# Kernel optimization log

Measured on AMD Instinct MI355X. Metric: run time of the kernel, lower is better.

The kernel has to match this reference:

```python
import jax, jax.numpy as jnp
import numpy as np

HEADS = 16
DIM_HEAD = 64
SCALE = DIM_HEAD ** -0.5
STEP = 0.6

def setup_inputs() -> dict:
    key = jax.random.key(0)
    ks = jax.random.split(key, 8)
    B, N, QD = 2, 2048, 1024
    M, CD = 1024, 768
    inner = HEADS * DIM_HEAD  # 1024
    return {
        "x": jax.random.normal(ks[0], (B, N, QD), jnp.float32),
        "context": jax.random.normal(ks[1], (B, M, CD), jnp.float32),
        "focused_attention_mask": jax.random.uniform(ks[2], (1, M, M), jnp.float32),
        "Wq": jax.random.normal(ks[3], (inner, QD), jnp.float32) * 0.02,
        "Wk": jax.random.normal(ks[4], (inner, CD), jnp.float32) * 0.02,
        "Wv": jax.random.normal(ks[5], (inner, CD), jnp.float32) * 0.02,
        "Wo": jax.random.normal(ks[6], (QD, inner), jnp.float32) * 0.02,
        "bo": jax.random.normal(ks[7], (QD,), jnp.float32) * 0.02,
    }

def _split_heads(t, h):
    b, n, hd = t.shape
    return t.reshape(b, n, h, hd // h).transpose(0, 2, 1, 3).reshape(b * h, n, hd // h)

def reference(x, context, focused_attention_mask, Wq, Wk, Wv, Wo, bo):
    b, n, _ = x.shape
    h = HEADS
    q = _split_heads(x @ Wq.T, h)        # (b h) n d
    k = _split_heads(context @ Wk.T, h)  # (b h) m d
    v = _split_heads(context @ Wv.T, h)
    sim = jnp.einsum('bid,bjd->bij', q, k) * SCALE  # (b h) n m
    # FCA focus-weight modulation (fam has leading dim 1, broadcast over b*h)
    fam = focused_attention_mask[0]  # (m, m)
    K = fam.shape[-1]
    fw = jnp.abs(jnp.einsum('bqk,dk->bqd', sim[:, :, :K], fam))  # (b h) n m
    fw = jnp.minimum(fw, 1.0)
    fw = fw / (jnp.max(fw, axis=2, keepdims=True) + 1e-6)
    fw = (fw > STEP).astype(sim.dtype)
    sim = sim.at[:, :, :K].add((fw - 1.0) * 50.0)
    attn = jax.nn.softmax(sim, axis=-1)
    out = jnp.einsum('bij,bjd->bid', attn, v)  # (b h) n d
    out = out.reshape(b, h, n, -1).transpose(0, 2, 1, 3).reshape(b, n, -1)
    return out @ Wo.T + bo
```

## Files before the change

### kernel.cpp

```cpp
#include <hip/hip_runtime.h>
#include <hip/hip_fp16.h>
#include <math.h>

#define SCALE 0.125f

typedef _Float16 f16;
typedef __attribute__((ext_vector_type(8))) _Float16 f16x8;
typedef __attribute__((ext_vector_type(4))) float f32x4;

#define MFMA(a, b, c) __builtin_amdgcn_mfma_f32_16x16x32_f16((a), (b), (c), 0, 0, 0)

#define LX(r, qd) (((r) << 6) + ((((qd) ^ ((r) & 7))) << 3))

__device__ __forceinline__ void gll16(const f16* g, f16* l) {
    __builtin_amdgcn_global_load_lds(
        (const __attribute__((address_space(1))) unsigned int*)(g),
        (__attribute__((address_space(3))) unsigned int*)(l),
        16, 0, 0);
}

struct SplitSeg { const float* src; f16* h; f16* l; float scale; size_t n; };
struct SplitArgs { SplitSeg seg[7]; };

__global__ __launch_bounds__(256) void split_all(SplitArgs a)
{
    SplitSeg s = a.seg[blockIdx.y];
    size_t i4 = ((size_t)blockIdx.x * 256 + threadIdx.x) * 4;
    size_t stride = (size_t)gridDim.x * 256 * 4;
    for (; i4 < s.n; i4 += stride) {
        float4 v = *(const float4*)&s.src[i4];
        float av[4] = {v.x * s.scale, v.y * s.scale, v.z * s.scale, v.w * s.scale};
        f16 hv[4], lv[4];
#pragma unroll
        for (int j = 0; j < 4; ++j) {
            hv[j] = (f16)av[j];
            lv[j] = (f16)(av[j] - (float)hv[j]);
        }
        *(float2*)&s.h[i4] = *(float2*)hv;
        *(float2*)&s.l[i4] = *(float2*)lv;
    }
}

template <int AP, int BP>
__global__ __launch_bounds__(256) void gemm16(
    const f16* __restrict__ Ah, const f16* __restrict__ Al, size_t Abat,
    const f16* __restrict__ Bh, const f16* __restrict__ Bl, int Bstr, size_t Bbat,
    float* __restrict__ Cf, const float* __restrict__ bias,
    f16* __restrict__ Ch, f16* __restrict__ Cl, int Cpitch,
    f16* __restrict__ Cth, f16* __restrict__ Ctl, int Mt,
    int Nsplit, f16* __restrict__ C2th, int Mt2,
    size_t Cbat, float oscale, int M, int N, int K)
{
    constexpr int NCH = AP * 16 + BP * 8;
    __shared__ __align__(16) f16 Ash[AP][128 * 64];
    __shared__ __align__(16) f16 Bsh[BP][64 * 64];

    const int tid  = threadIdx.x;
    const int z    = blockIdx.z;
    Ah += z * Abat; if (AP == 2) Al += z * Abat;
    Bh += z * Bbat; if (BP == 2) Bl += z * Bbat;
    const int m0   = blockIdx.y * 128;
    const int n0   = blockIdx.x * 64;
    const int w    = tid >> 6;
    const int lane = tid & 63;
    const int wm   = (w >> 1) * 64;
    const int wn   = (w & 1) * 32;
    const int lq   = lane >> 4;
    const int l15  = lane & 15;
    const int sr   = lane >> 3;
    const int sg   = lane & 7;

    f32x4 acc[4][2];
#pragma unroll
    for (int mi = 0; mi < 4; ++mi)
#pragma unroll
        for (int ni = 0; ni < 2; ++ni) acc[mi][ni] = (f32x4){0.f, 0.f, 0.f, 0.f};

    for (int k0 = 0; k0 < K; k0 += 64) {
        __syncthreads();
#pragma unroll
        for (int c = 0; c < NCH / 4; ++c) {
            int chunk = c * 4 + w;
            const f16* gp; f16* lp;
            if (chunk < AP * 16) {
                int pl = chunk >> 4, sub = chunk & 15;
                int r = sub * 8 + sr;
                int g = sg ^ (r & 7);
                gp = ((AP == 2 && pl) ? Al : Ah) + (size_t)(m0 + r) * K + k0 + g * 8;
                lp = &Ash[pl][sub * 512];
            } else {
                int cb = chunk - AP * 16;
                int pl = cb >> 3, sub = cb & 7;
                int r = sub * 8 + sr;
                int g = sg ^ (r & 7);
                gp = ((BP == 2 && pl) ? Bl : Bh) + (size_t)(n0 + r) * Bstr + k0 + g * 8;
                lp = &Bsh[pl][sub * 512];
            }
            gll16(gp, lp);
        }
        __syncthreads();

#pragma unroll
        for (int kc = 0; kc < 2; ++kc) {
            f16x8 afh[4], afl[4];
#pragma unroll
            for (int mi = 0; mi < 4; ++mi) {
                int r = wm + mi * 16 + l15;
                afh[mi] = *(const f16x8*)&Ash[0][LX(r, kc * 4 + lq)];
                if (AP == 2) afl[mi] = *(const f16x8*)&Ash[1][LX(r, kc * 4 + lq)];
            }
#pragma unroll
            for (int ni = 0; ni < 2; ++ni) {
                int r = wn + ni * 16 + l15;
                f16x8 bh = *(const f16x8*)&Bsh[0][LX(r, kc * 4 + lq)];
                f16x8 bl;
                if (BP == 2) bl = *(const f16x8*)&Bsh[1][LX(r, kc * 4 + lq)];
#pragma unroll
                for (int mi = 0; mi < 4; ++mi) {
                    f32x4 a = acc[mi][ni];
                    a = MFMA(afh[mi], bh, a);
                    if (BP == 2) a = MFMA(afh[mi], bl, a);
                    if (AP == 2) a = MFMA(afl[mi], bh, a);
                    acc[mi][ni] = a;
                }
            }
        }
    }

    const bool vhalf = (Nsplit > 0) && (n0 >= Nsplit);
    if (Cf)  Cf  += z * Cbat;
    if (Ch)  { Ch += z * Cbat; if (Cl) Cl += z * Cbat; }

#pragma unroll
    for (int mi = 0; mi < 4; ++mi) {
#pragma unroll
        for (int ni = 0; ni < 2; ++ni) {
            int row = m0 + wm + mi * 16 + lq * 4;
            int col = n0 + wn + ni * 16 + l15;
            float v[4];
#pragma unroll
            for (int r = 0; r < 4; ++r) v[r] = acc[mi][ni][r] * oscale;
            if (Cf) {
                float bb = bias ? bias[col] : 0.f;
#pragma unroll
                for (int r = 0; r < 4; ++r)
                    Cf[(size_t)(row + r) * Cpitch + col] = v[r] + bb;
            } else if (vhalf) {
                union { f16 a[4]; float2 f; } uh;
#pragma unroll
                for (int r = 0; r < 4; ++r) uh.a[r] = (f16)v[r];
                *(float2*)&C2th[(size_t)(col - Nsplit) * Mt2 + row] = uh.f;
            } else {
                if (Ch) {
#pragma unroll
                    for (int r = 0; r < 4; ++r) {
                        f16 hh = (f16)v[r];
                        Ch[(size_t)(row + r) * Cpitch + col] = hh;
                        if (Cl) Cl[(size_t)(row + r) * Cpitch + col] = (f16)(v[r] - (float)hh);
                    }
                }
                if (Cth) {
                    union { f16 a[4]; float2 f; } uh, ul;
#pragma unroll
                    for (int r = 0; r < 4; ++r) {
                        uh.a[r] = (f16)v[r];
                        ul.a[r] = (f16)(v[r] - (float)uh.a[r]);
                    }
                    *(float2*)&Cth[(size_t)col * Mt + row] = uh.f;
                    if (Ctl) *(float2*)&Ctl[(size_t)col * Mt + row] = ul.f;
                }
            }
        }
    }
}

__global__ __launch_bounds__(512) void attn_mfma(
    const f16* __restrict__ Qh, const f16* __restrict__ Ql,
    const f16* __restrict__ Kh,
    const f16* __restrict__ Gh, const f16* __restrict__ Gl,
    const f16* __restrict__ Vth, f16* __restrict__ AOh)
{
    __shared__ __align__(16) f16 Ksh[2][4096];
    __shared__ __align__(16) f16 Gsh[2][2][4096];
    __shared__ __align__(16) f16 Vsh[4096];
    __shared__ __align__(16) f16 Ps[128 * 72];
    __shared__ int eflag[8];

    const int tid = threadIdx.x;
    const int bh = blockIdx.x;
    const int b = bh >> 4, h = bh & 15;
    const int qr0 = blockIdx.y * 128;
    const int w = tid >> 6, lane = tid & 63;
    const int lq = lane >> 4, l15 = lane & 15;
    const int wq = w * 16;

    const size_t qb = ((size_t)(b * 2048 + qr0)) * 1024 + h * 64;
    const size_t kb = ((size_t)(b * 1024)) * 1024 + h * 64;
    const size_t vb = (size_t)(h * 64) * 2048 + b * 1024;

    const int sr = lane >> 3;
    const int ss = lane & 7;

    f16x8 aqh[2], aql[2];
#pragma unroll
    for (int kc = 0; kc < 2; ++kc) {
        size_t off = qb + (size_t)(wq + l15) * 1024 + (kc * 4 + lq) * 8;
        aqh[kc] = *(const f16x8*)&Qh[off];
        aql[kc] = *(const f16x8*)&Ql[off];
    }

    float mx[4] = {};
    for (int jt = 0; jt < 16; ++jt) {
#pragma unroll
        for (int c = 0; c < 2; ++c) {
            int chunk = c * 8 + w;
            int pl = chunk >> 3, sub = chunk & 7;
            int r = sub * 8 + sr;
            int g = ss ^ (r & 7);
            const f16* gp = (pl ? Gl : Gh) + kb + (size_t)(jt * 64 + r) * 1024 + g * 8;
            gll16(gp, &Gsh[0][pl][sub * 512]);
        }
        __syncthreads();

#pragma unroll
        for (int tj = 0; tj < 4; ++tj) {
            f32x4 a0 = {0.f, 0.f, 0.f, 0.f};
#pragma unroll
            for (int kc = 0; kc < 2; ++kc) {
                int lx = LX(tj * 16 + l15, kc * 4 + lq);
                f16x8 bgh = *(const f16x8*)&Gsh[0][0][lx];
                f16x8 bgl = *(const f16x8*)&Gsh[0][1][lx];
                a0 = MFMA(aqh[kc], bgh, a0);
                a0 = MFMA(aqh[kc], bgl, a0);
                a0 = MFMA(aql[kc], bgh, a0);
            }
#pragma unroll
            for (int r = 0; r < 4; ++r)
                mx[r] = fmaxf(mx[r], fminf(fabsf(a0[r] * SCALE), 1.f));
        }
        bool done = true;
#pragma unroll
        for (int r = 0; r < 4; ++r) {
            float m = mx[r];
#pragma unroll
            for (int d = 1; d < 16; d <<= 1)
                m = fmaxf(m, __shfl_xor(m, d, 64));
            mx[r] = m;
            done = done && (m >= 1.0f);
        }
        int wd = __all(done ? 1 : 0);
        if (lane == 0) eflag[w] = wd;
        __syncthreads();
        bool allw = true;
#pragma unroll
        for (int i = 0; i < 8; ++i) allw = allw && (eflag[i] != 0);
        if (allw) break;
    }
    float T[4];
#pragma unroll
    for (int r = 0; r < 4; ++r)
        T[r] = 4.8f * (mx[r] + 1e-6f);

    const float SL2E = 0.125f * 1.44269504088896f;
    const float PEN2 = -50.0f * 1.44269504088896f;
    f32x4 aco[4];
#pragma unroll
    for (int dj = 0; dj < 4; ++dj) aco[dj] = (f32x4){0.f, 0.f, 0.f, 0.f};
    float dsum[4] = {};

    auto stageKG = [&](int jtn, int buf) {
#pragma unroll
        for (int c = 0; c < 3; ++c) {
            int chunk = c * 8 + w;
            int sub = chunk & 7;
            int r = sub * 8 + sr;
            int g = ss ^ (r & 7);
            size_t off = kb + (size_t)(jtn * 64 + r) * 1024 + g * 8;
            const f16* gp; f16* lp;
            if (chunk < 8)       { gp = Kh + off; lp = &Ksh[buf][sub * 512]; }
            else if (chunk < 16) { gp = Gh + off; lp = &Gsh[buf][0][sub * 512]; }
            else                 { gp = Gl + off; lp = &Gsh[buf][1][sub * 512]; }
            gll16(gp, lp);
        }
    };

    stageKG(0, 0);

    for (int jt = 0; jt < 16; ++jt) {
        const int cur = jt & 1;

        {
            int sub = w;
            int r = sub * 8 + sr;
            int g = ss ^ (r & 7);
            const f16* gp = Vth + vb + (size_t)r * 2048 + jt * 64 + g * 8;
            gll16(gp, &Vsh[sub * 512]);
        }
        if (jt < 15) {
            stageKG(jt + 1, cur ^ 1);
            asm volatile("s_waitcnt vmcnt(4)" ::: "memory");
        } else {
            asm volatile("s_waitcnt vmcnt(1)" ::: "memory");
        }
        __builtin_amdgcn_sched_barrier(0);
        __builtin_amdgcn_s_barrier();
        __builtin_amdgcn_sched_barrier(0);

#pragma unroll
        for (int tj = 0; tj < 4; ++tj) {
            f32x4 s0 = {0.f, 0.f, 0.f, 0.f}, f0 = {0.f, 0.f, 0.f, 0.f};
            __builtin_amdgcn_s_setprio(1);
#pragma unroll
            for (int kc = 0; kc < 2; ++kc) {
                int lx = LX(tj * 16 + l15, kc * 4 + lq);
                f16x8 bkh = *(const f16x8*)&Ksh[cur][lx];
                f16x8 bgh = *(const f16x8*)&Gsh[cur][0][lx];
                f16x8 bgl = *(const f16x8*)&Gsh[cur][1][lx];
                s0 = MFMA(aqh[kc], bkh, s0);
                f0 = MFMA(aqh[kc], bgh, f0);
                f0 = MFMA(aqh[kc], bgl, f0);
                f0 = MFMA(aql[kc], bgh, f0);
            }
            __builtin_amdgcn_s_setprio(0);
#pragma unroll
            for (int r = 0; r < 4; ++r) {
                float p0 = (fabsf(f0[r]) > T[r]) ? 0.f : PEN2;
                f16 e0 = (f16)exp2f(fmaf(s0[r], SL2E, p0));
                Ps[(wq + lq * 4 + r) * 72 + tj * 16 + l15] = e0;
                dsum[r] += (float)e0;
            }
        }

        if (jt < 15) asm volatile("s_waitcnt vmcnt(3)" ::: "memory");
        else         asm volatile("s_waitcnt vmcnt(0)" ::: "memory");
        asm volatile("s_waitcnt lgkmcnt(0)" ::: "memory");
        __builtin_amdgcn_sched_barrier(0);
        __builtin_amdgcn_s_barrier();
        __builtin_amdgcn_sched_barrier(0);

        __builtin_amdgcn_s_setprio(1);
#pragma unroll
        for (int kc = 0; kc < 2; ++kc) {
            f16x8 ap = *(const f16x8*)&Ps[(wq + l15) * 72 + kc * 32 + lq * 8];
#pragma unroll
            for (int dj = 0; dj < 4; ++dj) {
                int lx = LX(dj * 16 + l15, kc * 4 + lq);
                f16x8 bvh = *(const f16x8*)&Vsh[lx];
                aco[dj] = MFMA(ap, bvh, aco[dj]);
            }
        }
        __builtin_amdgcn_s_setprio(0);

        asm volatile("s_waitcnt lgkmcnt(0)" ::: "memory");
        __builtin_amdgcn_sched_barrier(0);
        __builtin_amdgcn_s_barrier();
        __builtin_amdgcn_sched_barrier(0);
    }

#pragma unroll
    for (int r = 0; r < 4; ++r) {
        float s = dsum[r];
#pragma unroll
        for (int d = 1; d < 16; d <<= 1)
            s += __shfl_xor(s, d, 64);
        dsum[r] = s;
    }
#pragma unroll
    for (int r = 0; r < 4; ++r) {
        float invd = 1.0f / dsum[r];
        int qq = qr0 + wq + lq * 4 + r;
#pragma unroll
        for (int dj = 0; dj < 4; ++dj) {
            int dd = h * 64 + dj * 16 + l15;
            AOh[(size_t)(b * 2048 + qq) * 1024 + dd] = (f16)(aco[dj][r] * invd);
        }
    }
}

extern "C" void kernel_launch(void* const* d_in, const int* in_sizes, int n_in,
                              void* d_out, int out_size, void* d_ws, size_t ws_size,
                              hipStream_t stream)
{
    const float* x   = (const float*)d_in[0];
    const float* ctx = (const float*)d_in[1];
    const float* fam = (const float*)d_in[2];
    const float* Wq  = (const float*)d_in[3];
    const float* Wk  = (const float*)d_in[4];
    const float* Wv  = (const float*)d_in[5];
    const float* Wo  = (const float*)d_in[6];
    const float* bo  = (const float*)d_in[7];
    float* out = (float*)d_out;

    const size_t nX  = (size_t)4096 * 1024;
    const size_t nC  = (size_t)2048 * 768;
    const size_t nWq = (size_t)1024 * 1024;
    const size_t nWk = (size_t)1024 * 768;
    const size_t nF  = (size_t)1024 * 1024;
    const size_t nK  = (size_t)2048 * 1024;

    char* p = (char*)d_ws;
    f16 *xh   = (f16*)p; p += nX * 2;   f16 *xl   = (f16*)p; p += nX * 2;
    f16 *ch   = (f16*)p; p += nC * 2;   f16 *cl   = (f16*)p; p += nC * 2;
    f16 *wqh  = (f16*)p; p += nWq * 2;  f16 *wql  = (f16*)p; p += nWq * 2;
    f16 *wkvh = (f16*)p; p += nWk * 4;  f16 *wkvl = (f16*)p; p += nWk * 4;
    f16 *woh  = (f16*)p; p += nWq * 2;  f16 *wol  = (f16*)p; p += nWq * 2;
    f16 *fmh  = (f16*)p; p += nF * 2;   f16 *fml  = (f16*)p; p += nF * 2;
    f16 *qh   = (f16*)p; p += nX * 2;   f16 *ql   = (f16*)p; p += nX * 2;
    f16 *kh   = (f16*)p; p += nK * 2;
    f16 *kth  = (f16*)p; p += nK * 2;   f16 *ktl  = (f16*)p; p += nK * 2;
    f16 *vth  = (f16*)p; p += nK * 2;
    f16 *gh   = (f16*)p; p += nK * 2;   f16 *gl   = (f16*)p; p += nK * 2;
    f16 *aoh  = (f16*)p; p += nX * 2;

    const float WS  = 64.0f;
    const float IWS = 1.0f / 64.0f;

    SplitArgs sa;
    sa.seg[0] = {x,   xh,          xl,          1.f, nX};
    sa.seg[1] = {ctx, ch,          cl,          1.f, nC};
    sa.seg[2] = {Wq,  wqh,         wql,         WS,  nWq};
    sa.seg[3] = {Wk,  wkvh,        wkvl,        WS,  nWk};
    sa.seg[4] = {Wv,  wkvh + nWk,  wkvl + nWk,  WS,  nWk};
    sa.seg[5] = {Wo,  woh,         wol,         WS,  nWq};
    sa.seg[6] = {fam, fmh,         fml,         1.f, nF};
    split_all<<<dim3(64, 7), 256, 0, stream>>>(sa);

    gemm16<2, 2><<<dim3(16, 32, 1), 256, 0, stream>>>(
        xh, xl, 0, wqh, wql, 1024, 0,
        nullptr, nullptr, qh, ql, 1024, nullptr, nullptr, 0,
        0, nullptr, 0, 0, IWS, 4096, 1024, 1024);

    gemm16<2, 2><<<dim3(32, 16, 1), 256, 0, stream>>>(
        ch, cl, 0, wkvh, wkvl, 768, 0,
        nullptr, nullptr, kh, nullptr, 1024, kth, ktl, 2048,
        1024, vth, 2048, 0, IWS, 2048, 2048, 768);

    gemm16<2, 2><<<dim3(16, 8, 2), 256, 0, stream>>>(
        fmh, fml, 0, kth, ktl, 2048, 1024,
        nullptr, nullptr, gh, gl, 1024, nullptr, nullptr, 0,
        0, nullptr, 0, (size_t)1024 * 1024, 1.f, 1024, 1024, 1024);

    attn_mfma<<<dim3(32, 16), 512, 0, stream>>>(qh, ql, kh, gh, gl, vth, aoh);

    gemm16<1, 1><<<dim3(16, 32, 1), 256, 0, stream>>>(
        aoh, nullptr, 0, woh, nullptr, 1024, 0,
        out, bo, nullptr, nullptr, 1024, nullptr, nullptr, 0,
        0, nullptr, 0, 0, IWS, 4096, 1024, 1024);
}
```

Measured before the change: 276.3 us.

## Switch attention to 32x32 MFMA with transposed scores kept in registers

Rewrites the attention kernel to use 32x32x16 MFMA. Each pair of waves now covers 32 query rows and splits the 64-key tile in half, computing transposed S^T/F^T tiles so the probabilities can be repacked into A-operand fragments with cross-half shuffles instead of going through an LDS P buffer. The two key-halves' output partials and row sums are combined through shared memory at the end. This aims to cut LDS traffic and per-MFMA overhead, at the cost of an extra cross-wave reduction step and different register pressure; it also adds a launch_bounds occupancy hint.

```diff
diff --git a/kernel.cpp b/kernel.cpp
--- a/kernel.cpp
+++ b/kernel.cpp
@@ -7,16 +7,28 @@
 typedef _Float16 f16;
 typedef __attribute__((ext_vector_type(8))) _Float16 f16x8;
 typedef __attribute__((ext_vector_type(4))) float f32x4;
-
-#define MFMA(a, b, c) __builtin_amdgcn_mfma_f32_16x16x32_f16((a), (b), (c), 0, 0, 0)
+typedef __attribute__((ext_vector_type(16))) float f32x16;
+
+#define MFMA(a, b, c)   __builtin_amdgcn_mfma_f32_16x16x32_f16((a), (b), (c), 0, 0, 0)
+#define MFMA32(a, b, c) __builtin_amdgcn_mfma_f32_32x32x16_f16((a), (b), (c), 0, 0, 0)
 
 #define LX(r, qd) (((r) << 6) + ((((qd) ^ ((r) & 7))) << 3))
+
+#define CROW(e, hi) (((e) & 3) + 8 * ((e) >> 2) + 4 * (hi))
 
 __device__ __forceinline__ void gll16(const f16* g, f16* l) {
     __builtin_amdgcn_global_load_lds(
         (const __attribute__((address_space(1))) unsigned int*)(g),
         (__attribute__((address_space(3))) unsigned int*)(l),
         16, 0, 0);
+}
+
+union U8 { unsigned u[4]; f16x8 v; };
+
+__device__ __forceinline__ unsigned pkrtz(float a, float b) {
+    unsigned r;
+    asm("v_cvt_pkrtz_f16_f32 %0, %1, %2" : "=v"(r) : "v"(a), "v"(b));
+    return r;
 }
 
 struct SplitSeg { const float* src; f16* h; f16* l; float scale; size_t n; };
@@ -174,7 +186,7 @@
     }
 }
 
-__global__ __launch_bounds__(512) void attn_mfma(
+__global__ __launch_bounds__(512, 4) void attn_mfma(
     const f16* __restrict__ Qh, const f16* __restrict__ Ql,
     const f16* __restrict__ Kh,
     const f16* __restrict__ Gh, const f16* __restrict__ Gl,
@@ -183,7 +195,7 @@
     __shared__ __align__(16) f16 Ksh[2][4096];
     __shared__ __align__(16) f16 Gsh[2][2][4096];
     __shared__ __align__(16) f16 Vsh[4096];
-    __shared__ __align__(16) f16 Ps[128 * 72];
+    __shared__ float mxsh[4][2][32];
     __shared__ int eflag[8];
 
     const int tid = threadIdx.x;
@@ -191,8 +203,10 @@
     const int b = bh >> 4, h = bh & 15;
     const int qr0 = blockIdx.y * 128;
     const int w = tid >> 6, lane = tid & 63;
-    const int lq = lane >> 4, l15 = lane & 15;
-    const int wq = w * 16;
+    const int l31 = lane & 31, hi = lane >> 5;
+    const int wq = w >> 1;
+    const int wk = w & 1;
+    const int arow = wk * 32 + l31;
 
     const size_t qb = ((size_t)(b * 2048 + qr0)) * 1024 + h * 64;
     const size_t kb = ((size_t)(b * 1024)) * 1024 + h * 64;
@@ -201,15 +215,15 @@
     const int sr = lane >> 3;
     const int ss = lane & 7;
 
-    f16x8 aqh[2], aql[2];
-#pragma unroll
-    for (int kc = 0; kc < 2; ++kc) {
-        size_t off = qb + (size_t)(wq + l15) * 1024 + (kc * 4 + lq) * 8;
-        aqh[kc] = *(const f16x8*)&Qh[off];
-        aql[kc] = *(const f16x8*)&Ql[off];
-    }
-
-    float mx[4] = {};
+    f16x8 bqh[4], bql[4];
+#pragma unroll
+    for (int c = 0; c < 4; ++c) {
+        size_t off = qb + (size_t)(wq * 32 + l31) * 1024 + c * 16 + hi * 8;
+        bqh[c] = *(const f16x8*)&Qh[off];
+        bql[c] = *(const f16x8*)&Ql[off];
+    }
+
+    float mxr = 0.f, rowmax = 0.f;
     for (int jt = 0; jt < 16; ++jt) {
 #pragma unroll
         for (int c = 0; c < 2; ++c) {
@@ -217,38 +231,31 @@
             int pl = chunk >> 3, sub = chunk & 7;
             int r = sub * 8 + sr;
             int g = ss ^ (r & 7);
-            const f16* gp = (pl ? Gl : Gh) + kb + (size_t)(jt * 64 + r) * 1024 + g * 8;
-            gll16(gp, &Gsh[0][pl][sub * 512]);
+            gll16((pl ? Gl : Gh) + kb + (size_t)(jt * 64 + r) * 1024 + g * 8,
+                  &Gsh[0][pl][sub * 512]);
         }
         __syncthreads();
 
-#pragma unroll
-        for (int tj = 0; tj < 4; ++tj) {
-            f32x4 a0 = {0.f, 0.f, 0.f, 0.f};
-#pragma unroll
-            for (int kc = 0; kc < 2; ++kc) {
-                int lx = LX(tj * 16 + l15, kc * 4 + lq);
-                f16x8 bgh = *(const f16x8*)&Gsh[0][0][lx];
-                f16x8 bgl = *(const f16x8*)&Gsh[0][1][lx];
-                a0 = MFMA(aqh[kc], bgh, a0);
-                a0 = MFMA(aqh[kc], bgl, a0);
-                a0 = MFMA(aql[kc], bgh, a0);
-            }
-#pragma unroll
-            for (int r = 0; r < 4; ++r)
-                mx[r] = fmaxf(mx[r], fminf(fabsf(a0[r] * SCALE), 1.f));
-        }
-        bool done = true;
-#pragma unroll
-        for (int r = 0; r < 4; ++r) {
-            float m = mx[r];
-#pragma unroll
-            for (int d = 1; d < 16; d <<= 1)
-                m = fmaxf(m, __shfl_xor(m, d, 64));
-            mx[r] = m;
-            done = done && (m >= 1.0f);
-        }
-        int wd = __all(done ? 1 : 0);
+        f32x16 fw;
+#pragma unroll
+        for (int e = 0; e < 16; ++e) fw[e] = 0.f;
+#pragma unroll
+        for (int c = 0; c < 4; ++c) {
+            int lx = LX(arow, c * 2 + hi);
+            f16x8 agh = *(const f16x8*)&Gsh[0][0][lx];
+            f16x8 agl = *(const f16x8*)&Gsh[0][1][lx];
+            fw = MFMA32(agh, bqh[c], fw);
+            fw = MFMA32(agh, bql[c], fw);
+            fw = MFMA32(agl, bqh[c], fw);
+        }
+#pragma unroll
+        for (int e = 0; e < 16; ++e)
+            mxr = fmaxf(mxr, fminf(fabsf(fw[e]) * SCALE, 1.f));
+        float m2 = fmaxf(mxr, __shfl_xor(mxr, 32, 64));
+        if (lane < 32) mxsh[wq][wk][lane] = m2;
+        __syncthreads();
+        rowmax = fmaxf(m2, mxsh[wq][wk ^ 1][l31]);
+        int wd = __all((rowmax >= 1.0f) ? 1 : 0);
         if (lane == 0) eflag[w] = wd;
         __syncthreads();
         bool allw = true;
@@ -256,17 +263,16 @@
         for (int i = 0; i < 8; ++i) allw = allw && (eflag[i] != 0);
         if (allw) break;
     }
-    float T[4];
-#pragma unroll
-    for (int r = 0; r < 4; ++r)
-        T[r] = 4.8f * (mx[r] + 1e-6f);
+    const float T = 4.8f * (rowmax + 1e-6f);
 
     const float SL2E = 0.125f * 1.44269504088896f;
     const float PEN2 = -50.0f * 1.44269504088896f;
-    f32x4 aco[4];
-#pragma unroll
-    for (int dj = 0; dj < 4; ++dj) aco[dj] = (f32x4){0.f, 0.f, 0.f, 0.f};
-    float dsum[4] = {};
+    f32x16 aco[2];
+#pragma unroll
+    for (int dt = 0; dt < 2; ++dt)
+#pragma unroll
+        for (int e = 0; e < 16; ++e) aco[dt][e] = 0.f;
+    float dsum = 0.f;
 
     auto stageKG = [&](int jtn, int buf) {
 #pragma unroll
@@ -290,11 +296,9 @@
         const int cur = jt & 1;
 
         {
-            int sub = w;
-            int r = sub * 8 + sr;
+            int r = w * 8 + sr;
             int g = ss ^ (r & 7);
-            const f16* gp = Vth + vb + (size_t)r * 2048 + jt * 64 + g * 8;
-            gll16(gp, &Vsh[sub * 512]);
+            gll16(Vth + vb + (size_t)r * 2048 + jt * 64 + g * 8, &Vsh[w * 512]);
         }
         if (jt < 15) {
             stageKG(jt + 1, cur ^ 1);
@@ -306,29 +310,45 @@
         __builtin_amdgcn_s_barrier();
         __builtin_amdgcn_sched_barrier(0);
 
-#pragma unroll
-        for (int tj = 0; tj < 4; ++tj) {
-            f32x4 s0 = {0.f, 0.f, 0.f, 0.f}, f0 = {0.f, 0.f, 0.f, 0.f};
-            __builtin_amdgcn_s_setprio(1);
-#pragma unroll
-            for (int kc = 0; kc < 2; ++kc) {
-                int lx = LX(tj * 16 + l15, kc * 4 + lq);
-                f16x8 bkh = *(const f16x8*)&Ksh[cur][lx];
-                f16x8 bgh = *(const f16x8*)&Gsh[cur][0][lx];
-                f16x8 bgl = *(const f16x8*)&Gsh[cur][1][lx];
-                s0 = MFMA(aqh[kc], bkh, s0);
-                f0 = MFMA(aqh[kc], bgh, f0);
-                f0 = MFMA(aqh[kc], bgl, f0);
-                f0 = MFMA(aql[kc], bgh, f0);
-            }
-            __builtin_amdgcn_s_setprio(0);
-#pragma unroll
-            for (int r = 0; r < 4; ++r) {
-                float p0 = (fabsf(f0[r]) > T[r]) ? 0.f : PEN2;
-                f16 e0 = (f16)exp2f(fmaf(s0[r], SL2E, p0));
-                Ps[(wq + lq * 4 + r) * 72 + tj * 16 + l15] = e0;
-                dsum[r] += (float)e0;
-            }
+        f32x16 s, f;
+#pragma unroll
+        for (int e = 0; e < 16; ++e) { s[e] = 0.f; f[e] = 0.f; }
+        __builtin_amdgcn_s_setprio(1);
+#pragma unroll
+        for (int c = 0; c < 4; ++c) {
+            int lx = LX(arow, c * 2 + hi);
+            f16x8 ak  = *(const f16x8*)&Ksh[cur][lx];
+            f16x8 agh = *(const f16x8*)&Gsh[cur][0][lx];
+            f16x8 agl = *(const f16x8*)&Gsh[cur][1][lx];
+            s = MFMA32(ak,  bqh[c], s);
+            f = MFMA32(agh, bqh[c], f);
+            f = MFMA32(agh, bql[c], f);
+            f = MFMA32(agl, bqh[c], f);
+        }
+        __builtin_amdgcn_s_setprio(0);
+
+#pragma unroll
+        for (int e = 0; e < 16; ++e) {
+            float pen = (fabsf(f[e]) > T) ? 0.f : PEN2;
+            float pe = exp2f(fmaf(s[e], SL2E, pen));
+            s[e] = pe;
+            dsum += pe;
+        }
+        f16x8 pa[2];
+#pragma unroll
+        for (int lc = 0; lc < 2; ++lc) {
+            unsigned w0 = pkrtz(s[8 * lc + 0], s[8 * lc + 1]);
+            unsigned w1 = pkrtz(s[8 * lc + 2], s[8 * lc + 3]);
+            unsigned w2 = pkrtz(s[8 * lc + 4], s[8 * lc + 5]);
+            unsigned w3 = pkrtz(s[8 * lc + 6], s[8 * lc + 7]);
+            unsigned r0 = (unsigned)__shfl_xor((int)(hi ? w0 : w2), 32, 64);
+            unsigned r1 = (unsigned)__shfl_xor((int)(hi ? w1 : w3), 32, 64);
+            U8 fr;
+            fr.u[0] = hi ? r0 : w0;
+            fr.u[1] = hi ? r1 : w1;
+            fr.u[2] = hi ? w2 : r0;
+            fr.u[3] = hi ? w3 : r1;
+            pa[lc] = fr.v;
         }
 
         if (jt < 15) asm volatile("s_waitcnt vmcnt(3)" ::: "memory");
@@ -340,13 +360,11 @@
 
         __builtin_amdgcn_s_setprio(1);
 #pragma unroll
-        for (int kc = 0; kc < 2; ++kc) {
-            f16x8 ap = *(const f16x8*)&Ps[(wq + l15) * 72 + kc * 32 + lq * 8];
-#pragma unroll
-            for (int dj = 0; dj < 4; ++dj) {
-                int lx = LX(dj * 16 + l15, kc * 4 + lq);
-                f16x8 bvh = *(const f16x8*)&Vsh[lx];
-                aco[dj] = MFMA(ap, bvh, aco[dj]);
+        for (int lc = 0; lc < 2; ++lc) {
+#pragma unroll
+            for (int dt = 0; dt < 2; ++dt) {
+                f16x8 bv = *(const f16x8*)&Vsh[LX(dt * 32 + l31, (wk * 2 + lc) * 2 + hi)];
+                aco[dt] = MFMA32(pa[lc], bv, aco[dt]);
             }
         }
         __builtin_amdgcn_s_setprio(0);
@@ -357,23 +375,31 @@
         __builtin_amdgcn_sched_barrier(0);
     }
 
-#pragma unroll
-    for (int r = 0; r < 4; ++r) {
-        float s = dsum[r];
-#pragma unroll
-        for (int d = 1; d < 16; d <<= 1)
-            s += __shfl_xor(s, d, 64);
-        dsum[r] = s;
-    }
-#pragma unroll
-    for (int r = 0; r < 4; ++r) {
-        float invd = 1.0f / dsum[r];
-        int qq = qr0 + wq + lq * 4 + r;
-#pragma unroll
-        for (int dj = 0; dj < 4; ++dj) {
-            int dd = h * 64 + dj * 16 + l15;
-            AOh[(size_t)(b * 2048 + qq) * 1024 + dd] = (f16)(aco[dj][r] * invd);
-        }
+    float dsum2 = dsum + __shfl_xor(dsum, 32, 64);
+    float* Osh = (float*)&Gsh[0][0][0];
+    if (wk == 0) {
+#pragma unroll
+        for (int dt = 0; dt < 2; ++dt)
+#pragma unroll
+            for (int e = 0; e < 16; ++e)
+                Osh[(wq * 32 + CROW(e, hi)) * 64 + dt * 32 + l31] = aco[dt][e];
+        if (lane < 32) mxsh[wq][0][lane] = dsum2;
+    }
+    __syncthreads();
+    if (wk == 1) {
+        float inv = 1.0f / (dsum2 + mxsh[wq][0][l31]);
+        float iv[16];
+#pragma unroll
+        for (int e = 0; e < 16; ++e) iv[e] = __shfl(inv, CROW(e, hi), 64);
+#pragma unroll
+        for (int dt = 0; dt < 2; ++dt)
+#pragma unroll
+            for (int e = 0; e < 16; ++e) {
+                int qq = wq * 32 + CROW(e, hi);
+                float o = aco[dt][e] + Osh[qq * 64 + dt * 32 + l31];
+                AOh[(size_t)(b * 2048 + qr0 + qq) * 1024 + h * 64 + dt * 32 + l31]
+                    = (f16)(o * iv[e]);
+            }
     }
 }
 
```

New measurement: 291.8 us. 5.6% more time.
